# Kernel tuning notes

Hardware: AMD Instinct MI355X
Metric: run time of the kernel (lower is better)

## Reference

```python
import jax, jax.numpy as jnp
import numpy as np

D_MODEL = 1024
HEAD_SIZE = 64

def setup_inputs() -> dict:
    key = jax.random.key(0)
    ks = jax.random.split(key, 7)
    s = 1.0 / np.sqrt(D_MODEL)
    x = jax.random.normal(ks[0], (4, 4096, D_MODEL), dtype=jnp.float32)
    Wq = jax.random.uniform(ks[1], (D_MODEL, HEAD_SIZE), jnp.float32, -s, s)
    bq = jax.random.uniform(ks[2], (HEAD_SIZE,), jnp.float32, -s, s)
    Wk = jax.random.uniform(ks[3], (D_MODEL, HEAD_SIZE), jnp.float32, -s, s)
    bk = jax.random.uniform(ks[4], (HEAD_SIZE,), jnp.float32, -s, s)
    Wv = jax.random.uniform(ks[5], (D_MODEL, HEAD_SIZE), jnp.float32, -s, s)
    bv = jax.random.uniform(ks[6], (HEAD_SIZE,), jnp.float32, -s, s)
    return {"x": x, "Wq": Wq, "bq": bq, "Wk": Wk, "bk": bk, "Wv": Wv, "bv": bv}

def reference(x, Wq, bq, Wk, bk, Wv, bv):
    # x: [B, S, D]; projections to [B, S, H]
    Q = jnp.einsum('bsd,dh->bsh', x, Wq) + bq
    K = jnp.einsum('bsd,dh->bsh', x, Wk) + bk
    V = jnp.einsum('bsd,dh->bsh', x, Wv) + bv
    scores = jnp.einsum('bqh,bkh->bqk', Q, K) / jnp.sqrt(jnp.float32(HEAD_SIZE))
    attn = jax.nn.softmax(scores, axis=-1)  # [B, S, S]
    return jnp.einsum('bqk,bkh->bqh', attn, V)
```

## Files before the change

kernel.cpp:

```cpp
#include <hip/hip_runtime.h>
#include <hip/hip_bf16.h>


#define S_LEN 4096
#define D_MODEL 1024

typedef __attribute__((ext_vector_type(8))) short bf16x8;
typedef __attribute__((ext_vector_type(4))) float f32x4;
typedef __attribute__((ext_vector_type(16))) float f32x16;

__device__ inline short f2bf(float f) {
    union { float f; unsigned u; } v;
    v.f = f;
    unsigned r = v.u + 0x7fffu + ((v.u >> 16) & 1u);
    return (short)(r >> 16);
}

__device__ inline unsigned cvt_pk(float lo, float hi) {
    unsigned r;
    asm("v_cvt_pk_bf16_f32 %0, %1, %2" : "=v"(r) : "v"(lo), "v"(hi));
    return r;
}

__device__ inline void pl32swap(unsigned& a, unsigned& b) {
    asm("v_permlane32_swap_b32 %0, %1" : "+v"(a), "+v"(b));
}

__device__ inline f32x16 fzero16() {
    f32x16 z;
#pragma unroll
    for (int i = 0; i < 16; ++i) z[i] = 0.f;
    return z;
}

__device__ inline void gload_lds16(const void* g, void* l) {
    __builtin_amdgcn_global_load_lds((const __attribute__((address_space(1))) void*)g,
                                     (__attribute__((address_space(3))) void*)l, 16, 0, 0);
}

__global__ void prep_w(const float* __restrict__ Wq, const float* __restrict__ Wk,
                       const float* __restrict__ Wv, short* __restrict__ WtF) {
    int idx = blockIdx.x * 256 + threadIdx.x;
    int j = idx & 7;
    int lane = (idx >> 3) & 63;
    int f = idx >> 9;
    int ntg = f % 12;
    int kb = f / 12;
    int k = (kb >> 1) * 64 + (kb & 1) * 32 + (lane >> 4) * 8 + j;
    int c = ntg * 16 + (lane & 15);
    const float* W = (c < 64) ? Wq : (c < 128 ? Wk : Wv);
    WtF[idx] = f2bf(W[k * 64 + (c & 63)]);
}

__launch_bounds__(512)
__global__ void proj_kernel(const float* __restrict__ x, const short* __restrict__ WtF,
                            const float* __restrict__ bq, const float* __restrict__ bk,
                            const float* __restrict__ bv,
                            short* __restrict__ Qb, short* __restrict__ Kb,
                            short* __restrict__ Vt) {
    __shared__ __align__(16) char bsm[2 * 24576];
    __shared__ short vsm[64][72];
    const float CEXP = 0.18033688011112042f;
    int w = threadIdx.x >> 6;
    int lane = threadIdx.x & 63;
    int g = lane >> 4, ln = lane & 15;
    int rt = w >> 1, nh = w & 1;
    int rowbase = blockIdx.x * 64;

    const char* WtB = (const char*)WtF;

    auto stageW = [&](int buf, int bkt) {
#pragma unroll
        for (int i = 0; i < 3; ++i) {
            const char* src = WtB + (size_t)bkt * 24576 + w * 3072 + i * 1024 + lane * 16;
            gload_lds16(src, bsm + buf * 24576 + w * 3072 + i * 1024);
        }
    };

    f32x4 acc[6];
#pragma unroll
    for (int i = 0; i < 6; ++i) acc[i] = (f32x4){0.f, 0.f, 0.f, 0.f};

    const float* xw = x + (size_t)(rowbase + rt * 16 + ln) * D_MODEL + g * 8;

    stageW(0, 0);
    f32x4 A0 = *(const f32x4*)(xw);
    f32x4 A1 = *(const f32x4*)(xw + 4);
    f32x4 A2 = *(const f32x4*)(xw + 32);
    f32x4 A3 = *(const f32x4*)(xw + 36);
    __syncthreads();

    int cur = 0;
#pragma unroll 1
    for (int bkt = 0; bkt < 16; ++bkt) {
        f32x4 N0, N1, N2, N3;
        if (bkt < 15) {
            const float* xn = xw + (bkt + 1) * 64;
            N0 = *(const f32x4*)(xn);
            N1 = *(const f32x4*)(xn + 4);
            N2 = *(const f32x4*)(xn + 32);
            N3 = *(const f32x4*)(xn + 36);
            stageW(cur ^ 1, bkt + 1);
        }
        const char* bs = bsm + cur * 24576;
        {
            union { bf16x8 v; unsigned u[4]; } A;
            A.u[0] = cvt_pk(A0[0], A0[1]);
            A.u[1] = cvt_pk(A0[2], A0[3]);
            A.u[2] = cvt_pk(A1[0], A1[1]);
            A.u[3] = cvt_pk(A1[2], A1[3]);
#pragma unroll
            for (int nt = 0; nt < 6; ++nt) {
                bf16x8 bfr = *(const bf16x8*)(bs + (nh * 6 + nt) * 1024 + lane * 16);
                acc[nt] = __builtin_amdgcn_mfma_f32_16x16x32_bf16(A.v, bfr, acc[nt], 0, 0, 0);
            }
        }
        {
            union { bf16x8 v; unsigned u[4]; } A;
            A.u[0] = cvt_pk(A2[0], A2[1]);
            A.u[1] = cvt_pk(A2[2], A2[3]);
            A.u[2] = cvt_pk(A3[0], A3[1]);
            A.u[3] = cvt_pk(A3[2], A3[3]);
#pragma unroll
            for (int nt = 0; nt < 6; ++nt) {
                bf16x8 bfr = *(const bf16x8*)(bs + (12 + nh * 6 + nt) * 1024 + lane * 16);
                acc[nt] = __builtin_amdgcn_mfma_f32_16x16x32_bf16(A.v, bfr, acc[nt], 0, 0, 0);
            }
        }
        __syncthreads();
        if (bkt < 15) { A0 = N0; A1 = N1; A2 = N2; A3 = N3; }
        cur ^= 1;
    }

#pragma unroll
    for (int nt = 0; nt < 6; ++nt) {
        int c = nh * 96 + nt * 16 + ln;
        int proj = c >> 6;
        int h = c & 63;
        float bias = (proj == 0 ? bq : (proj == 1 ? bk : bv))[h];
#pragma unroll
        for (int r = 0; r < 4; ++r) {
            int srow = rowbase + rt * 16 + g * 4 + r;
            float v = acc[nt][r] + bias;
            if (proj == 0) v *= CEXP;
            short hv = f2bf(v);
            if (proj == 0) {
                Qb[(size_t)srow * 64 + h] = hv;
            } else if (proj == 1) {
                Kb[(size_t)srow * 64 + h] = hv;
            } else {
                vsm[h][rt * 16 + g * 4 + r] = hv;
            }
        }
    }
    __syncthreads();
    {
        int t = threadIdx.x;
        int h = t >> 3, c = t & 7;
        bf16x8 val = *(const bf16x8*)&vsm[h][c * 8];
        int bb = rowbase >> 12;
        int sg = (rowbase & 4095) + c * 8;
        *(bf16x8*)(Vt + ((size_t)(bb * 64 + h) << 12) + sg) = val;
    }
}

__launch_bounds__(512)
__global__ void attn_kernel(const short* __restrict__ Qb, const short* __restrict__ Kb,
                            const short* __restrict__ Vt, float* __restrict__ out) {
    __shared__ __align__(16) char smraw[131072];
    __shared__ float lsm[256];
    int lane = threadIdx.x & 63;
    int w = threadIdx.x >> 6;
    int l31 = lane & 31, hi = lane >> 5;
    int sp = w >> 1, qt = w & 1;

    int bid = blockIdx.x;
    int sb = (bid & 7) * 32 + (bid >> 3);
    int b = sb >> 6, qs = sb & 63;
    size_t qrow0 = ((size_t)b << 12) + (size_t)qs * 64;

    char* base = smraw + sp * 32768;
    char* kbuf = base;
    char* vbuf = base + 16384;

    const char* KB = (const char*)(Kb + (((size_t)b << 12) + sp * 1024) * 64);
    const char* VB = (const char*)Vt + (((size_t)b * 64) << 13) + (size_t)sp * 2048;

    auto stageT = [&](int buf, int t) {
        if (qt == 0) {
            char* dst = kbuf + buf * 8192;
#pragma unroll
            for (int i = 0; i < 8; ++i) {
                int od = i * 1024 + lane * 16;
                int row = od >> 7, colb = od & 127;
                const char* src = KB + (size_t)(t * 64 + row) * 128 + (colb ^ ((row & 7) << 4));
                gload_lds16(src, dst + i * 1024);
            }
        } else {
            char* dst = vbuf + buf * 8192;
#pragma unroll
            for (int i = 0; i < 8; ++i) {
                int od = i * 1024 + lane * 16;
                int row = od >> 7, colb = od & 127;
                const char* src = VB + (size_t)row * 8192 + t * 128 + (colb ^ ((row & 7) << 4));
                gload_lds16(src, dst + i * 1024);
            }
        }
    };

    bf16x8 qf[4];
    {
        const short* qp = Qb + (qrow0 + qt * 32 + l31) * 64 + hi * 8;
#pragma unroll
        for (int ks = 0; ks < 4; ++ks) qf[ks] = *(const bf16x8*)(qp + ks * 16);
    }

    f32x16 oacc0 = fzero16(), oacc1 = fzero16();
    float lacc[16];
#pragma unroll
    for (int r = 0; r < 16; ++r) lacc[r] = 0.f;

    int swz = (l31 & 7) << 4;
    stageT(0, 0);

#pragma unroll 1
    for (int t = 0; t < 16; ++t) {
        asm volatile("s_waitcnt vmcnt(0)" ::: "memory");
        __builtin_amdgcn_s_barrier();
        __builtin_amdgcn_sched_barrier(0);
        if (t < 15) stageT((t + 1) & 1, t + 1);

        const char* kc = kbuf + (t & 1) * 8192;
        const char* vc = vbuf + (t & 1) * 8192;

        bf16x8 kf[8];
#pragma unroll
        for (int kt = 0; kt < 2; ++kt)
#pragma unroll
            for (int ks = 0; ks < 4; ++ks)
                kf[kt * 4 + ks] = *(const bf16x8*)(kc + (kt * 32 + l31) * 128
                                                  + ((ks * 32 + hi * 16) ^ swz));
        f32x16 s0 = fzero16(), s1 = fzero16();
#pragma unroll
        for (int ks = 0; ks < 4; ++ks) {
            s0 = __builtin_amdgcn_mfma_f32_32x32x16_bf16(kf[ks], qf[ks], s0, 0, 0, 0);
            s1 = __builtin_amdgcn_mfma_f32_32x32x16_bf16(kf[4 + ks], qf[ks], s1, 0, 0, 0);
        }

        bf16x8 vf[8];
#pragma unroll
        for (int ht = 0; ht < 2; ++ht)
#pragma unroll
            for (int kk = 0; kk < 4; ++kk)
                vf[ht * 4 + kk] = *(const bf16x8*)(vc + (ht * 32 + l31) * 128
                                                   + ((kk * 32 + hi * 16) ^ swz));

        float p0[16], p1[16];
#pragma unroll
        for (int r = 0; r < 16; ++r) p0[r] = exp2f(s0[r]);
#pragma unroll
        for (int r = 0; r < 16; ++r) p1[r] = exp2f(s1[r]);
#pragma unroll
        for (int r = 0; r < 16; ++r) lacc[r] += p0[r] + p1[r];

        union { unsigned u[4]; bf16x8 v; } t00, t01, t10, t11;
        {
            unsigned D[8];
#pragma unroll
            for (int dw = 0; dw < 8; ++dw) D[dw] = cvt_pk(p0[2 * dw], p0[2 * dw + 1]);
            pl32swap(D[0], D[2]); pl32swap(D[1], D[3]);
            pl32swap(D[4], D[6]); pl32swap(D[5], D[7]);
            t00.u[0] = D[0]; t00.u[1] = D[1]; t00.u[2] = D[2]; t00.u[3] = D[3];
            t01.u[0] = D[4]; t01.u[1] = D[5]; t01.u[2] = D[6]; t01.u[3] = D[7];
        }
        {
            unsigned D[8];
#pragma unroll
            for (int dw = 0; dw < 8; ++dw) D[dw] = cvt_pk(p1[2 * dw], p1[2 * dw + 1]);
            pl32swap(D[0], D[2]); pl32swap(D[1], D[3]);
            pl32swap(D[4], D[6]); pl32swap(D[5], D[7]);
            t10.u[0] = D[0]; t10.u[1] = D[1]; t10.u[2] = D[2]; t10.u[3] = D[3];
            t11.u[0] = D[4]; t11.u[1] = D[5]; t11.u[2] = D[6]; t11.u[3] = D[7];
        }

        oacc0 = __builtin_amdgcn_mfma_f32_32x32x16_bf16(vf[0], t00.v, oacc0, 0, 0, 0);
        oacc1 = __builtin_amdgcn_mfma_f32_32x32x16_bf16(vf[4], t00.v, oacc1, 0, 0, 0);
        oacc0 = __builtin_amdgcn_mfma_f32_32x32x16_bf16(vf[1], t01.v, oacc0, 0, 0, 0);
        oacc1 = __builtin_amdgcn_mfma_f32_32x32x16_bf16(vf[5], t01.v, oacc1, 0, 0, 0);
        oacc0 = __builtin_amdgcn_mfma_f32_32x32x16_bf16(vf[2], t10.v, oacc0, 0, 0, 0);
        oacc1 = __builtin_amdgcn_mfma_f32_32x32x16_bf16(vf[6], t10.v, oacc1, 0, 0, 0);
        oacc0 = __builtin_amdgcn_mfma_f32_32x32x16_bf16(vf[3], t11.v, oacc0, 0, 0, 0);
        oacc1 = __builtin_amdgcn_mfma_f32_32x32x16_bf16(vf[7], t11.v, oacc1, 0, 0, 0);
    }

    float lfin;
    {
        float lt[8];
#pragma unroll
        for (int r = 0; r < 8; ++r) lt[r] = lacc[r] + lacc[r + 8];
#pragma unroll
        for (int st = 4; st >= 1; st >>= 1)
#pragma unroll
            for (int r = 0; r < 4; ++r)
                if (r < st) lt[r] += lt[r + st];
        lfin = lt[0] + __shfl_xor(lt[0], 32);
    }

    __syncthreads();
    float* osm = (float*)smraw;
    {
        float* ow = osm + (size_t)(w * 32 + l31) * 68;
#pragma unroll
        for (int r = 0; r < 16; ++r) {
            int h = (r & 3) + 8 * (r >> 2) + 4 * hi;
            ow[h] = oacc0[r];
            ow[32 + h] = oacc1[r];
        }
        if (hi == 0) lsm[w * 32 + l31] = lfin;
    }
    __syncthreads();
    {
        int tq = threadIdx.x >> 3, hb = (threadIdx.x & 7) * 8;
        int qt2 = tq >> 5, ql = tq & 31;
        f32x4 oa = (f32x4){0.f, 0.f, 0.f, 0.f}, ob = (f32x4){0.f, 0.f, 0.f, 0.f};
        float lsum = 0.f;
#pragma unroll
        for (int sp2 = 0; sp2 < 4; ++sp2) {
            int w2 = sp2 * 2 + qt2;
            lsum += lsm[w2 * 32 + ql];
            const float* src = osm + (size_t)(w2 * 32 + ql) * 68 + hb;
            f32x4 x0 = *(const f32x4*)src;
            f32x4 x1 = *(const f32x4*)(src + 4);
#pragma unroll
            for (int j = 0; j < 4; ++j) { oa[j] += x0[j]; ob[j] += x1[j]; }
        }
        float inv = 1.f / lsum;
        f32x4 r0, r1;
#pragma unroll
        for (int j = 0; j < 4; ++j) { r0[j] = oa[j] * inv; r1[j] = ob[j] * inv; }
        float* op = out + (qrow0 + tq) * 64 + hb;
        *(f32x4*)op = r0;
        *(f32x4*)(op + 4) = r1;
    }
}

extern "C" void kernel_launch(void* const* d_in, const int* in_sizes, int n_in,
                              void* d_out, int out_size, void* d_ws, size_t ws_size,
                              hipStream_t stream) {
    const float* x  = (const float*)d_in[0];
    const float* Wq = (const float*)d_in[1];
    const float* bq = (const float*)d_in[2];
    const float* Wk = (const float*)d_in[3];
    const float* bk = (const float*)d_in[4];
    const float* Wv = (const float*)d_in[5];
    const float* bv = (const float*)d_in[6];

    short* ws = (short*)d_ws;
    short* WtF = ws;
    short* Qb = WtF + 192 * 1024;
    short* Kb = Qb + 16384 * 64;
    short* Vt = Kb + 16384 * 64;

    prep_w<<<768, 256, 0, stream>>>(Wq, Wk, Wv, WtF);
    proj_kernel<<<256, 512, 0, stream>>>(x, WtF, bq, bk, bv, Qb, Kb, Vt);
    attn_kernel<<<256, 512, 0, stream>>>(Qb, Kb, Vt, (float*)d_out);
}
```

Before: 70.88 us.

## Stage x tiles into swizzled LDS with async loads in projection kernel

```diff
diff --git a/kernel.cpp b/kernel.cpp
--- a/kernel.cpp
+++ b/kernel.cpp
@@ -58,8 +58,7 @@
                             const float* __restrict__ bv,
                             short* __restrict__ Qb, short* __restrict__ Kb,
                             short* __restrict__ Vt) {
-    __shared__ __align__(16) char bsm[2 * 24576];
-    __shared__ short vsm[64][72];
+    __shared__ __align__(16) char smem[81920];
     const float CEXP = 0.18033688011112042f;
     int w = threadIdx.x >> 6;
     int lane = threadIdx.x & 63;
@@ -67,13 +66,26 @@
     int rt = w >> 1, nh = w & 1;
     int rowbase = blockIdx.x * 64;
 
+    char* xbuf = smem;
+    char* wbuf = smem + 32768;
+    const char* xB = (const char*)x;
     const char* WtB = (const char*)WtF;
 
+    auto stageX = [&](int buf, int bkt) {
+#pragma unroll
+        for (int i = 0; i < 2; ++i) {
+            int od = w * 2048 + i * 1024 + lane * 16;
+            int row = od >> 8, col = od & 255;
+            const char* src = xB + (size_t)(rowbase + row) * 4096 + bkt * 256
+                              + (col ^ ((row & 7) << 5));
+            gload_lds16(src, xbuf + buf * 16384 + w * 2048 + i * 1024);
+        }
+    };
     auto stageW = [&](int buf, int bkt) {
 #pragma unroll
         for (int i = 0; i < 3; ++i) {
             const char* src = WtB + (size_t)bkt * 24576 + w * 3072 + i * 1024 + lane * 16;
-            gload_lds16(src, bsm + buf * 24576 + w * 3072 + i * 1024);
+            gload_lds16(src, wbuf + buf * 24576 + w * 3072 + i * 1024);
         }
     };
 
@@ -81,61 +93,50 @@
 #pragma unroll
     for (int i = 0; i < 6; ++i) acc[i] = (f32x4){0.f, 0.f, 0.f, 0.f};
 
-    const float* xw = x + (size_t)(rowbase + rt * 16 + ln) * D_MODEL + g * 8;
-
+    stageX(0, 0);
     stageW(0, 0);
-    f32x4 A0 = *(const f32x4*)(xw);
-    f32x4 A1 = *(const f32x4*)(xw + 4);
-    f32x4 A2 = *(const f32x4*)(xw + 32);
-    f32x4 A3 = *(const f32x4*)(xw + 36);
-    __syncthreads();
-
-    int cur = 0;
+
+    int arow = rt * 16 + ln;
+    int aswz = (arow & 7) << 5;
+
 #pragma unroll 1
-    for (int bkt = 0; bkt < 16; ++bkt) {
-        f32x4 N0, N1, N2, N3;
-        if (bkt < 15) {
-            const float* xn = xw + (bkt + 1) * 64;
-            N0 = *(const f32x4*)(xn);
-            N1 = *(const f32x4*)(xn + 4);
-            N2 = *(const f32x4*)(xn + 32);
-            N3 = *(const f32x4*)(xn + 36);
-            stageW(cur ^ 1, bkt + 1);
-        }
-        const char* bs = bsm + cur * 24576;
-        {
+    for (int t = 0; t < 16; ++t) {
+        asm volatile("s_waitcnt vmcnt(0)" ::: "memory");
+        __builtin_amdgcn_s_barrier();
+        __builtin_amdgcn_sched_barrier(0);
+        if (t < 15) {
+            stageX((t + 1) & 1, t + 1);
+            stageW((t + 1) & 1, t + 1);
+        }
+        const char* xc = xbuf + (t & 1) * 16384;
+        const char* wc = wbuf + (t & 1) * 24576;
+
+#pragma unroll
+        for (int kk = 0; kk < 2; ++kk) {
+            int cb = (kk * 128 + g * 32) ^ aswz;
+            f32x4 X0 = *(const f32x4*)(xc + arow * 256 + cb);
+            f32x4 X1 = *(const f32x4*)(xc + arow * 256 + cb + 16);
             union { bf16x8 v; unsigned u[4]; } A;
-            A.u[0] = cvt_pk(A0[0], A0[1]);
-            A.u[1] = cvt_pk(A0[2], A0[3]);
-            A.u[2] = cvt_pk(A1[0], A1[1]);
-            A.u[3] = cvt_pk(A1[2], A1[3]);
+            A.u[0] = cvt_pk(X0[0], X0[1]);
+            A.u[1] = cvt_pk(X0[2], X0[3]);
+            A.u[2] = cvt_pk(X1[0], X1[1]);
+            A.u[3] = cvt_pk(X1[2], X1[3]);
 #pragma unroll
             for (int nt = 0; nt < 6; ++nt) {
-                bf16x8 bfr = *(const bf16x8*)(bs + (nh * 6 + nt) * 1024 + lane * 16);
+                int fr = kk * 12 + nh * 6 + nt;
+                bf16x8 bfr = *(const bf16x8*)(wc + fr * 1024 + lane * 16);
                 acc[nt] = __builtin_amdgcn_mfma_f32_16x16x32_bf16(A.v, bfr, acc[nt], 0, 0, 0);
             }
         }
-        {
-            union { bf16x8 v; unsigned u[4]; } A;
-            A.u[0] = cvt_pk(A2[0], A2[1]);
-            A.u[1] = cvt_pk(A2[2], A2[3]);
-            A.u[2] = cvt_pk(A3[0], A3[1]);
-            A.u[3] = cvt_pk(A3[2], A3[3]);
-#pragma unroll
-            for (int nt = 0; nt < 6; ++nt) {
-                bf16x8 bfr = *(const bf16x8*)(bs + (12 + nh * 6 + nt) * 1024 + lane * 16);
-                acc[nt] = __builtin_amdgcn_mfma_f32_16x16x32_bf16(A.v, bfr, acc[nt], 0, 0, 0);
-            }
-        }
-        __syncthreads();
-        if (bkt < 15) { A0 = N0; A1 = N1; A2 = N2; A3 = N3; }
-        cur ^= 1;
-    }
-
+    }
+
+    __syncthreads();
+    short* vsm = (short*)smem;
 #pragma unroll
     for (int nt = 0; nt < 6; ++nt) {
-        int c = nh * 96 + nt * 16 + ln;
-        int proj = c >> 6;
+        int ntg = nh * 6 + nt;
+        int c = ntg * 16 + ln;
+        int proj = ntg >> 2;
         int h = c & 63;
         float bias = (proj == 0 ? bq : (proj == 1 ? bk : bv))[h];
 #pragma unroll
@@ -149,7 +150,7 @@
             } else if (proj == 1) {
                 Kb[(size_t)srow * 64 + h] = hv;
             } else {
-                vsm[h][rt * 16 + g * 4 + r] = hv;
+                vsm[h * 72 + rt * 16 + g * 4 + r] = hv;
             }
         }
     }
@@ -157,7 +158,7 @@
     {
         int t = threadIdx.x;
         int h = t >> 3, c = t & 7;
-        bf16x8 val = *(const bf16x8*)&vsm[h][c * 8];
+        bf16x8 val = *(const bf16x8*)&vsm[h * 72 + c * 8];
         int bb = rowbase >> 12;
         int sg = (rowbase & 4095) + c * 8;
         *(bf16x8*)(Vt + ((size_t)(bb * 64 + h) << 12) + sg) = val;
```

Result: faster. 60.08 us (-15.2%).
